# Performance work log

Measured on AMD Instinct MI355X. Metric: run time of the kernel, lower is better.

Reference implementation:

```python
import jax, jax.numpy as jnp
from jax import lax
import numpy as np

NEG_SLOPE = 0.01  # nn.LeakyReLU default


def conv1d(x, w, b, stride=1, padding=0, groups=1):
    # x: (N, C, L), w: (O, C//groups, K), torch Conv1d semantics
    y = lax.conv_general_dilated(
        x, w, window_strides=(stride,), padding=[(padding, padding)],
        dimension_numbers=('NCH', 'OIH', 'NCH'), feature_group_count=groups)
    return y + b[None, :, None]


def maxpool1d_ceil(x, k, s):
    # torch max_pool1d with ceil_mode=True: window may overhang right edge
    L = x.shape[-1]
    out_len = -(-(L - k) // s) + 1  # ceil((L-k)/s)+1
    pad = max(0, (out_len - 1) * s + k - L)
    xp = jnp.pad(x, ((0, 0), (0, 0), (0, pad)), constant_values=-jnp.inf)
    return lax.reduce_window(xp, -jnp.inf, lax.max, (1, 1, k), (1, 1, s), 'VALID')


def adaptive_maxpool1d(x, out_size):
    # Spatial_LSTM_block.get_adaptive_pool (ceil_mode=False default)
    L = x.shape[-1]
    s = L // out_size
    k = L - (out_size - 1) * s
    return lax.reduce_window(x, -jnp.inf, lax.max, (1, 1, k), (1, 1, s), 'VALID')


def lstm_last_h(xseq, w_ih, b_ih, w_hh, b_hh):
    # xseq: (T, B, F); PyTorch LSTMCell gate order: i, f, g, o
    B = xseq.shape[1]
    H = w_hh.shape[1]
    h0 = jnp.zeros((B, H), dtype=xseq.dtype)
    c0 = jnp.zeros((B, H), dtype=xseq.dtype)

    def step(carry, xt):
        h, c = carry
        g = xt @ w_ih.T + b_ih + h @ w_hh.T + b_hh  # (B, 4H)
        i, f, gg, o = jnp.split(g, 4, axis=-1)
        c = jax.nn.sigmoid(f) * c + jax.nn.sigmoid(i) * jnp.tanh(gg)
        h = jax.nn.sigmoid(o) * jnp.tanh(c)
        return (h, c), None

    (h, _), _ = lax.scan(step, (h0, c0), xseq)
    return h


def setup_inputs() -> dict:
    ks = jax.random.split(jax.random.key(0), 32)
    def rn(i, shape, s=0.05):
        return jax.random.normal(ks[i], shape, dtype=jnp.float32) * s
    return {
        'X': jax.random.normal(ks[0], (64, 16, 4096), dtype=jnp.float32),
        # depthwise conv: 16 -> 16*16=256, k=30, groups=16
        'w_dw': rn(1, (256, 1, 30)), 'b_dw': rn(2, (256,)),
        # pointwise conv: 256 -> 32, k=1
        'w_pw': rn(3, (32, 256, 1)), 'b_pw': rn(4, (32,)),
        # conv2: 32 -> 64, k=10
        'w_c2': rn(5, (64, 32, 10)), 'b_c2': rn(6, (64,)),
        # pyramid branch 0 (bin=300): conv 64->4 k=3 p=1, LSTMCell(4,64), Linear(64,1)
        'w_sc0': rn(7, (4, 64, 3)), 'b_sc0': rn(8, (4,)),
        'w_ih0': rn(9, (256, 4)), 'b_ih0': rn(10, (256,)),
        'w_hh0': rn(11, (256, 64)), 'b_hh0': rn(12, (256,)),
        'w_lin0': rn(13, (1, 64)), 'b_lin0': rn(14, (1,)),
        # pyramid branch 1 (bin=100)
        'w_sc1': rn(15, (4, 64, 3)), 'b_sc1': rn(16, (4,)),
        'w_ih1': rn(17, (256, 4)), 'b_ih1': rn(18, (256,)),
        'w_hh1': rn(19, (256, 64)), 'b_hh1': rn(20, (256,)),
        'w_lin1': rn(21, (1, 64)), 'b_lin1': rn(22, (1,)),
        # final head: Linear(len(bins)=2 -> 1), sigmoid
        'w_rul': rn(23, (1, 2)), 'b_rul': rn(24, (1,)),
    }


def reference(X, w_dw, b_dw, w_pw, b_pw, w_c2, b_c2,
              w_sc0, b_sc0, w_ih0, b_ih0, w_hh0, b_hh0, w_lin0, b_lin0,
              w_sc1, b_sc1, w_ih1, b_ih1, w_hh1, b_hh1, w_lin1, b_lin1,
              w_rul, b_rul):
    PYRAMID_BINS = (300, 100)
    x = conv1d(X, w_dw, b_dw, groups=16)            # (B, 256, 4067)
    x = conv1d(x, w_pw, b_pw)                        # (B, 32, 4067)
    x = jax.nn.leaky_relu(x, NEG_SLOPE)
    x = maxpool1d_ceil(x, 20, 5)                     # (B, 32, 811)
    x = conv1d(x, w_c2, b_c2)                        # (B, 64, 802)
    x = jax.nn.leaky_relu(x, NEG_SLOPE)
    branches = [
        (w_sc0, b_sc0, w_ih0, b_ih0, w_hh0, b_hh0, w_lin0, b_lin0),
        (w_sc1, b_sc1, w_ih1, b_ih1, w_hh1, b_hh1, w_lin1, b_lin1),
    ]
    outs = []
    for bin_size, (wsc, bsc, wih, bih, whh, bhh, wl, bl) in zip(PYRAMID_BINS, branches):
        xp = adaptive_maxpool1d(x, bin_size)          # (B, 64, bin)
        xc = jax.nn.leaky_relu(conv1d(xp, wsc, bsc, padding=1), NEG_SLOPE)  # (B, 4, bin)
        seq = jnp.transpose(xc, (2, 0, 1))            # (T, B, 4)
        h = lstm_last_h(seq, wih, bih, whh, bhh)      # (B, 64)
        outs.append(h @ wl.T + bl)                    # (B, 1)
    y = jnp.concatenate(outs, axis=1)                 # (B, 2)
    return jax.nn.sigmoid(y @ w_rul.T + b_rul)        # (B, 1)
```

## Files before the change

### kernel.cpp

```cpp
#include <hip/hip_runtime.h>
#include <cstddef>


typedef __attribute__((ext_vector_type(8))) short bf16x8;
typedef __attribute__((ext_vector_type(4))) float f32x4;
typedef unsigned int uint32;

#define LOG2E 1.4426950408889634f

__device__ __forceinline__ unsigned short f2bf(float f) {
    unsigned u = __float_as_uint(f);
    u += 0x7fffu + ((u >> 16) & 1u);
    return (unsigned short)(u >> 16);
}
__device__ __forceinline__ float bf2f(unsigned short h) {
    return __uint_as_float(((unsigned)h) << 16);
}
__device__ __forceinline__ float exp2_(float x) {
#if __has_builtin(__builtin_amdgcn_exp2f)
    return __builtin_amdgcn_exp2f(x);
#else
    return __expf(0.6931471805599453f * x);
#endif
}
__device__ __forceinline__ float rcp2(float x) {
    return __builtin_amdgcn_rcpf(1.0f + exp2_(x));
}
__device__ __forceinline__ float sigm(float x) {
    return __builtin_amdgcn_rcpf(1.0f + __expf(-x));
}
__device__ __forceinline__ float leaky(float v) { return v >= 0.0f ? v : 0.01f * v; }

__global__ void prep_kernel(const float* __restrict__ w_dw, const float* __restrict__ b_dw,
                            const float* __restrict__ w_pw, const float* __restrict__ b_pw,
                            unsigned short* __restrict__ Wp1, float* __restrict__ b_eff) {
    const int bid = blockIdx.x, tid = threadIdx.x;
    if (bid < 15) {
        const int kc = bid;
        for (int it = 0; it < 4; ++it) {
            int idx = tid + it * 256;
            int n = idx >> 5, kp = idx & 31;
            int ch = kp & 15, kappa = kc * 2 + (kp >> 4);
            float s = 0.f;
            for (int j = 0; j < 16; ++j)
                s += w_pw[n * 256 + ch * 16 + j] * w_dw[(ch * 16 + j) * 30 + kappa];
            Wp1[(kc * 32 + n) * 32 + kp] = f2bf(s);
        }
    } else if (tid < 32) {
        float s = b_pw[tid];
        for (int c = 0; c < 256; ++c) s += w_pw[tid * 256 + c] * b_dw[c];
        b_eff[tid] = s;
    }
}

__global__ __launch_bounds__(256) void conv1p_kernel(const float* __restrict__ X,
        const unsigned short* __restrict__ Wp1, const float* __restrict__ b_eff,
        unsigned short* __restrict__ S2b, int* __restrict__ cnt) {
    const int b = blockIdx.y, tx = blockIdx.x, tid = threadIdx.x;
    if (tx == 0 && b == 0 && tid == 0) *cnt = 0;
    const int l0 = tx * 160;
    __shared__ __align__(16) unsigned short Wl[480 * 40];
    __shared__ __align__(16) unsigned short U[192 * 33];
    unsigned short* Xt = U;
    {
        const int4* s4 = (const int4*)Wp1;
        for (int j = tid; j < 1920; j += 256)
            *(int4*)((uint32*)Wl + (j >> 2) * 20 + (j & 3) * 4) = s4[j];
    }
    for (int i = tid; i < 896; i += 256) {
        int ch = i / 56, p4 = (i - ch * 56) * 4;
        int l = l0 + p4;
        float4 v = {0.f, 0.f, 0.f, 0.f};
        const float* xrow = X + ((size_t)b * 16 + ch) * 4096;
        if (l + 3 < 4096 && p4 + 3 < 221) {
            v = *(const float4*)(xrow + l);
        } else {
            float* vv = (float*)&v;
#pragma unroll
            for (int e = 0; e < 4; ++e) {
                int p = p4 + e, le = l + e;
                vv[e] = (p < 221 && le < 4096) ? xrow[le] : 0.f;
            }
        }
        unsigned short* dst = Xt + p4 * 24 + ch;
        dst[0] = f2bf(v.x); dst[24] = f2bf(v.y); dst[48] = f2bf(v.z); dst[72] = f2bf(v.w);
    }
    __syncthreads();
    const int w = tid >> 6, lane = tid & 63, quad = lane >> 4, l16 = lane & 15;
    const int ki = quad >> 1, ch0 = (quad & 1) * 8;
    f32x4 acc[3][2];
#pragma unroll
    for (int mi = 0; mi < 3; ++mi)
#pragma unroll
        for (int nt = 0; nt < 2; ++nt) acc[mi][nt] = (f32x4){0.f, 0.f, 0.f, 0.f};
#pragma unroll
    for (int kc = 0; kc < 15; ++kc) {
        bf16x8 B0 = *(const bf16x8*)(Wl + (kc * 32 + l16) * 40 + quad * 8);
        bf16x8 B1 = *(const bf16x8*)(Wl + (kc * 32 + 16 + l16) * 40 + quad * 8);
#pragma unroll
        for (int mi = 0; mi < 3; ++mi) {
            int mrow = (w + mi * 4) * 16 + l16 + 2 * kc + ki;
            bf16x8 A = *(const bf16x8*)(Xt + mrow * 24 + ch0);
            acc[mi][0] = __builtin_amdgcn_mfma_f32_16x16x32_bf16(A, B0, acc[mi][0], 0, 0, 0);
            acc[mi][1] = __builtin_amdgcn_mfma_f32_16x16x32_bf16(A, B1, acc[mi][1], 0, 0, 0);
        }
    }
    __syncthreads();
    unsigned short* Ct = U;
#pragma unroll
    for (int mi = 0; mi < 3; ++mi) {
        int lrow = (w + mi * 4) * 16 + quad * 4;
#pragma unroll
        for (int nt = 0; nt < 2; ++nt) {
            int o = nt * 16 + l16;
            float be = b_eff[o];
#pragma unroll
            for (int r = 0; r < 4; ++r)
                Ct[(lrow + r) * 33 + o] = f2bf(leaky(acc[mi][nt][r] + be));
        }
    }
    __syncthreads();
    for (int idx = tid; idx < 1024; idx += 256) {
        int ti = idx >> 5, ch = idx & 31;
        int t = tx * 32 + ti;
        if (t < 811) {
            int pmax = 4067 - 5 * t; if (pmax > 20) pmax = 20;
            int pbase = 5 * ti;
            float m = bf2f(Ct[pbase * 33 + ch]);
            for (int p = 1; p < pmax; ++p) m = fmaxf(m, bf2f(Ct[(pbase + p) * 33 + ch]));
            S2b[((size_t)b * 32 + ch) * 812 + t] = f2bf(m);
        }
    }
}

__global__ __launch_bounds__(256) void conv2_kernel(const unsigned short* __restrict__ S2b,
        const float* __restrict__ w_c2, const float* __restrict__ b_c2,
        float* __restrict__ S3) {
    const int b = blockIdx.y, l0 = blockIdx.x * 64, tid = threadIdx.x;
    __shared__ __align__(16) unsigned short At[80 * 40];
    __shared__ __align__(16) unsigned short Wl[10 * 64 * 40];
    for (int pair = tid; pair < 2048; pair += 256) {
        int n = pair >> 5, kp = pair & 31;
        const float* src = w_c2 + n * 320 + kp * 10;
        unsigned short* dstc = Wl + n * 40 + kp;
#pragma unroll
        for (int kc = 0; kc < 10; ++kc) dstc[kc * 2560] = f2bf(src[kc]);
    }
    for (int i = tid; i < 2560; i += 256) {
        int ch = i / 80, p = i - ch * 80;
        int l = l0 + p;
        At[p * 40 + ch] = (p < 73 && l < 811)
            ? S2b[((size_t)b * 32 + ch) * 812 + l] : (unsigned short)0;
    }
    __syncthreads();
    const int w = tid >> 6, lane = tid & 63, quad = lane >> 4, l16 = lane & 15;
    const int mA = w * 16 + l16, ch0 = quad * 8;
    f32x4 acc[4];
#pragma unroll
    for (int nt = 0; nt < 4; ++nt) acc[nt] = (f32x4){0.f, 0.f, 0.f, 0.f};
#pragma unroll
    for (int kc = 0; kc < 10; ++kc) {
        bf16x8 A = *(const bf16x8*)(At + (mA + kc) * 40 + ch0);
#pragma unroll
        for (int nt = 0; nt < 4; ++nt) {
            bf16x8 Bf = *(const bf16x8*)(Wl + (kc * 64 + nt * 16 + l16) * 40 + quad * 8);
            acc[nt] = __builtin_amdgcn_mfma_f32_16x16x32_bf16(A, Bf, acc[nt], 0, 0, 0);
        }
    }
    const int lbase = l0 + w * 16 + quad * 4;
#pragma unroll
    for (int nt = 0; nt < 4; ++nt) {
        int o = nt * 16 + l16;
        float bc = b_c2[o];
#pragma unroll
        for (int r = 0; r < 4; ++r) {
            int l = lbase + r;
            if (l < 802) S3[((size_t)b * 64 + o) * 802 + l] = leaky(acc[nt][r] + bc);
        }
    }
}

__global__ __launch_bounds__(1024) void branch_kernel(const float* __restrict__ S3,
        const float* __restrict__ w_sc0, const float* __restrict__ b_sc0,
        const float* __restrict__ w_ih0, const float* __restrict__ b_ih0, const float* __restrict__ b_hh0,
        const float* __restrict__ w_sc1, const float* __restrict__ b_sc1,
        const float* __restrict__ w_ih1, const float* __restrict__ b_ih1, const float* __restrict__ b_hh1,
        float* __restrict__ Xg0, float* __restrict__ Xg1) {
    const int b = blockIdx.x, br = blockIdx.y;
    const int T = br ? 100 : 300;
    const float* w_sc = br ? w_sc1 : w_sc0;
    const float* b_sc = br ? b_sc1 : b_sc0;
    const float* w_ih = br ? w_ih1 : w_ih0;
    const float* b_ih = br ? b_ih1 : b_ih0;
    const float* b_hh = br ? b_hh1 : b_hh0;
    float* Xg = br ? Xg1 : Xg0;

    __shared__ float bufs[16][2][402];
    __shared__ unsigned short Ps[64][302];
    __shared__ float xcs[4][304];
    const int tid = threadIdx.x, wv = tid >> 6, lane = tid & 63;

    for (int ci = 0; ci < 4; ++ci) {
        const int c = wv * 4 + ci;
        const float* row = S3 + ((size_t)b * 64 + c) * 802;
        if (br == 0) {
            float* A = bufs[wv][0];
            float* B = bufs[wv][1];
            for (int it = 0; it < 7; ++it) {
                int q = lane + it * 64;
                if (q < 401) A[q] = fmaxf(row[2 * q], row[2 * q + 1]);
            }
            int len = 401;
#pragma unroll
            for (int sp = 1; sp <= 32; sp <<= 1) {
                int nl = len - sp;
                for (int it = 0; it < 7; ++it) {
                    int q = lane + it * 64;
                    if (q < nl) B[q] = fmaxf(A[q], A[q + sp]);
                }
                float* tmp = A; A = B; B = tmp; len = nl;
            }
            for (int it = 0; it < 5; ++it) {
                int t = lane + it * 64;
                if (t < 300) Ps[c][1 + t] = f2bf(fmaxf(A[t], A[t + 38]));
            }
            if (lane < 2) Ps[c][lane * 301] = 0;
        } else {
            for (int it = 0; it < 2; ++it) {
                int t = lane + it * 64;
                if (t < 100) {
                    float m = row[8 * t];
#pragma unroll
                    for (int p = 1; p < 10; ++p) m = fmaxf(m, row[8 * t + p]);
                    Ps[c][1 + t] = f2bf(m);
                }
            }
            if (lane < 2) Ps[c][lane * 101] = 0;
        }
    }
    __syncthreads();
    for (int i = tid; i < 4 * T; i += 1024) {
        int o = i / T, t = i - o * T;
        float sum = b_sc[o];
        const float* wvp = w_sc + o * 192;
        for (int c = 0; c < 64; ++c) {
            float p0 = bf2f(Ps[c][t]), p1 = bf2f(Ps[c][t + 1]), p2 = bf2f(Ps[c][t + 2]);
            sum += wvp[c * 3] * p0 + wvp[c * 3 + 1] * p1 + wvp[c * 3 + 2] * p2;
        }
        xcs[o][t] = leaky(sum);
    }
    __syncthreads();
    {
        const int n = tid & 255, tq = tid >> 8;
        const int g = n >> 6;
        const float sc = (g == 2) ? (-2.0f * LOG2E) : (-LOG2E);
        const float4 w4 = *(const float4*)(w_ih + n * 4);
        const float bias = b_ih[n] + b_hh[n];
        const int bt = b >> 2, q = b & 3;
        const int hidx = n & 63;
        const int wv2 = hidx >> 4, l16 = hidx & 15;
        const size_t off0 = ((((size_t)bt * 4 + wv2) * 4 + q) * 16 + l16) * 4 + g;
        for (int t = tq; t < T; t += 4) {
            float v = bias + w4.x * xcs[0][t] + w4.y * xcs[1][t]
                           + w4.z * xcs[2][t] + w4.w * xcs[3][t];
            Xg[(size_t)t * 16384 + off0] = sc * v;
        }
    }
}

#define HPAD 72
__global__ __launch_bounds__(256) void lstm_kernel(
    const float* __restrict__ Xg0, const float* __restrict__ Xg1,
    const float* __restrict__ Whh0, const float* __restrict__ Whh1,
    const float* __restrict__ wl0, const float* __restrict__ bl0,
    const float* __restrict__ wl1, const float* __restrict__ bl1,
    float* __restrict__ brbuf, int* __restrict__ cnt,
    const float* __restrict__ w_rul, const float* __restrict__ b_rul,
    float* __restrict__ out) {
    const int bt = blockIdx.x;
    const int br = blockIdx.y;
    const int T = (br == 0) ? 300 : 100;
    const float* Xg = (br == 0) ? Xg0 : Xg1;
    const float* Whh = (br == 0) ? Whh0 : Whh1;
    const float* wl = (br == 0) ? wl0 : wl1;
    const float* bl = (br == 0) ? bl0 : bl1;
    const float C2L = -2.0f * LOG2E;

    __shared__ __align__(16) unsigned short h_lds[2][16][HPAD];
    __shared__ int lastf;

    const int tid = threadIdx.x;
    const int w = tid >> 6, lane = tid & 63, quad = lane >> 4, l16 = lane & 15;
    const int hidx = w * 16 + l16;

    bf16x8 Bf[4][2];
#pragma unroll
    for (int g = 0; g < 4; ++g) {
        const int n = g * 64 + hidx;
        const float scg = (g == 2) ? (-2.0f * LOG2E) : (-LOG2E);
#pragma unroll
        for (int kc = 0; kc < 2; ++kc) {
            const float* src = Whh + n * 64 + kc * 32 + quad * 8;
            bf16x8 v;
#pragma unroll
            for (int j = 0; j < 8; ++j) v[j] = (short)f2bf(src[j] * scg);
            Bf[g][kc] = v;
        }
    }

    for (int i = tid; i < 2 * 16 * HPAD; i += 256) (&h_lds[0][0][0])[i] = 0;

    const float* xp = Xg + (((size_t)bt * 4 + w) * 4 + quad) * 64 + l16 * 4;

    f32x4 xb0 = *(const f32x4*)(xp);
    f32x4 xb1 = *(const f32x4*)(xp + 16384);

    float c0 = 0.f;

    __syncthreads();

    auto step = [&](int t, f32x4& xb) {
        const unsigned short* hrow = &h_lds[t & 1][l16][0];
        bf16x8 A0 = *(const bf16x8*)(hrow + quad * 8);
        bf16x8 A1 = *(const bf16x8*)(hrow + 32 + quad * 8);
        const f32x4 z = {0.f, 0.f, 0.f, 0.f};
        f32x4 ac[4];
#pragma unroll
        for (int g = 0; g < 4; ++g) {
            ac[g] = __builtin_amdgcn_mfma_f32_16x16x32_bf16(A0, Bf[g][0], z, 0, 0, 0);
            ac[g] = __builtin_amdgcn_mfma_f32_16x16x32_bf16(A1, Bf[g][1], ac[g], 0, 0, 0);
        }
        float iv = rcp2(ac[0][0] + xb[0]);
        float fv = rcp2(ac[1][0] + xb[1]);
        float gv = 2.0f * rcp2(ac[2][0] + xb[2]) - 1.0f;
        float ov = rcp2(ac[3][0] + xb[3]);
        if (t + 2 < T) xb = *(const f32x4*)(xp + (size_t)(t + 2) * 16384);
        float cs = fv * c0 + iv * gv;
        c0 = cs;
        float th = 2.0f * rcp2(cs * C2L) - 1.0f;
        h_lds[(t + 1) & 1][quad * 4][hidx] = f2bf(ov * th);
        __syncthreads();
    };

    for (int t = 0; t < T; t += 2) {
        step(t, xb0);
        step(t + 1, xb1);
    }

    if (tid < 4) {
        const unsigned short* hrow = &h_lds[0][tid * 4][0];
        float s = bl[0];
        for (int j = 0; j < 64; ++j) s += bf2f(hrow[j]) * wl[j];
        atomicExch(&brbuf[br * 64 + bt * 4 + tid], s);
    }
    __syncthreads();
    __threadfence();
    if (tid == 0) {
        int old = atomicAdd(cnt, 1);
        lastf = (old == 31);
    }
    __syncthreads();
    if (lastf) {
        __threadfence();
        if (tid < 64) {
            float v0 = atomicAdd(&brbuf[tid], 0.0f);
            float v1 = atomicAdd(&brbuf[64 + tid], 0.0f);
            float v = w_rul[0] * v0 + w_rul[1] * v1 + b_rul[0];
            out[tid] = sigm(v);
        }
    }
}

extern "C" void kernel_launch(void* const* d_in, const int* in_sizes, int n_in,
                              void* d_out, int out_size, void* d_ws, size_t ws_size,
                              hipStream_t stream) {
    const float* X     = (const float*)d_in[0];
    const float* w_dw  = (const float*)d_in[1];
    const float* b_dw  = (const float*)d_in[2];
    const float* w_pw  = (const float*)d_in[3];
    const float* b_pw  = (const float*)d_in[4];
    const float* w_c2  = (const float*)d_in[5];
    const float* b_c2  = (const float*)d_in[6];
    const float* w_sc0 = (const float*)d_in[7];
    const float* b_sc0 = (const float*)d_in[8];
    const float* w_ih0 = (const float*)d_in[9];
    const float* b_ih0 = (const float*)d_in[10];
    const float* w_hh0 = (const float*)d_in[11];
    const float* b_hh0 = (const float*)d_in[12];
    const float* w_l0  = (const float*)d_in[13];
    const float* b_l0  = (const float*)d_in[14];
    const float* w_sc1 = (const float*)d_in[15];
    const float* b_sc1 = (const float*)d_in[16];
    const float* w_ih1 = (const float*)d_in[17];
    const float* b_ih1 = (const float*)d_in[18];
    const float* w_hh1 = (const float*)d_in[19];
    const float* b_hh1 = (const float*)d_in[20];
    const float* w_l1  = (const float*)d_in[21];
    const float* b_l1  = (const float*)d_in[22];
    const float* w_rul = (const float*)d_in[23];
    const float* b_rul = (const float*)d_in[24];

    float* ws = (float*)d_ws;
    float* Xg0 = ws;
    float* Xg1 = ws + 4915200;
    unsigned short* S2b = (unsigned short*)(ws + 6553600);
    float* S3    = ws + 7385088;
    unsigned short* Wp1 = (unsigned short*)(ws + 10670080);
    float* b_eff = ws + 10677760;
    float* brbuf = ws + 10677792;
    int*   cnt   = (int*)(ws + 10677920);

    prep_kernel<<<16, 256, 0, stream>>>(w_dw, b_dw, w_pw, b_pw, Wp1, b_eff);
    conv1p_kernel<<<dim3(26, 64), 256, 0, stream>>>(X, Wp1, b_eff, S2b, cnt);
    conv2_kernel<<<dim3(13, 64), 256, 0, stream>>>(S2b, w_c2, b_c2, S3);
    branch_kernel<<<dim3(64, 2), 1024, 0, stream>>>(
        S3, w_sc0, b_sc0, w_ih0, b_ih0, b_hh0,
            w_sc1, b_sc1, w_ih1, b_ih1, b_hh1, Xg0, Xg1);
    lstm_kernel<<<dim3(16, 2), 256, 0, stream>>>(Xg0, Xg1, w_hh0, w_hh1,
                                                 w_l0, b_l0, w_l1, b_l1,
                                                 brbuf, cnt, w_rul, b_rul, (float*)d_out);
}
```

Measured before the change: 344.7 us.

## Interleave two independent batch tiles per LSTM block to hide MFMA latency

Each LSTM workgroup now carries two 4-sample batch tiles through the recurrence together. It issues their MFMAs interleaved so the two independent dependency chains overlap, and shares one barrier per timestep. The grid is halved to 8x2 blocks, the completion counter threshold drops accordingly, and the input-gate prefetch depth goes from 2 to 4 timesteps. This trades parallelism across CUs for better latency hiding within the serial recurrence, and raises register pressure.

```diff
diff --git a/kernel.cpp b/kernel.cpp
--- a/kernel.cpp
+++ b/kernel.cpp
@@ -277,7 +277,7 @@
     float* __restrict__ brbuf, int* __restrict__ cnt,
     const float* __restrict__ w_rul, const float* __restrict__ b_rul,
     float* __restrict__ out) {
-    const int bt = blockIdx.x;
+    const int btp = blockIdx.x;
     const int br = blockIdx.y;
     const int T = (br == 0) ? 300 : 100;
     const float* Xg = (br == 0) ? Xg0 : Xg1;
@@ -286,7 +286,7 @@
     const float* bl = (br == 0) ? bl0 : bl1;
     const float C2L = -2.0f * LOG2E;
 
-    __shared__ __align__(16) unsigned short h_lds[2][16][HPAD];
+    __shared__ __align__(16) unsigned short h_lds[2][2][16][HPAD];
     __shared__ int lastf;
 
     const int tid = threadIdx.x;
@@ -308,56 +308,79 @@
         }
     }
 
-    for (int i = tid; i < 2 * 16 * HPAD; i += 256) (&h_lds[0][0][0])[i] = 0;
-
-    const float* xp = Xg + (((size_t)bt * 4 + w) * 4 + quad) * 64 + l16 * 4;
-
-    f32x4 xb0 = *(const f32x4*)(xp);
-    f32x4 xb1 = *(const f32x4*)(xp + 16384);
-
-    float c0 = 0.f;
-
-    __syncthreads();
-
-    auto step = [&](int t, f32x4& xb) {
-        const unsigned short* hrow = &h_lds[t & 1][l16][0];
-        bf16x8 A0 = *(const bf16x8*)(hrow + quad * 8);
-        bf16x8 A1 = *(const bf16x8*)(hrow + 32 + quad * 8);
+    for (int i = tid; i < 2 * 2 * 16 * HPAD; i += 256) (&h_lds[0][0][0][0])[i] = 0;
+
+    const float* xp0 = Xg + ((((size_t)(2 * btp)) * 4 + w) * 4 + quad) * 64 + l16 * 4;
+    const float* xp1 = xp0 + 1024;
+
+    f32x4 xq0[4], xq1[4];
+#pragma unroll
+    for (int j = 0; j < 4; ++j) {
+        xq0[j] = *(const f32x4*)(xp0 + (size_t)j * 16384);
+        xq1[j] = *(const f32x4*)(xp1 + (size_t)j * 16384);
+    }
+
+    float c0 = 0.f, c1 = 0.f;
+
+    __syncthreads();
+
+    auto stepPair = [&](int t, f32x4& xa, f32x4& xb) {
+        const unsigned short* h0 = &h_lds[0][t & 1][l16][0];
+        const unsigned short* h1 = &h_lds[1][t & 1][l16][0];
+        bf16x8 A00 = *(const bf16x8*)(h0 + quad * 8);
+        bf16x8 A01 = *(const bf16x8*)(h0 + 32 + quad * 8);
+        bf16x8 A10 = *(const bf16x8*)(h1 + quad * 8);
+        bf16x8 A11 = *(const bf16x8*)(h1 + 32 + quad * 8);
         const f32x4 z = {0.f, 0.f, 0.f, 0.f};
-        f32x4 ac[4];
+        f32x4 ac0[4], ac1[4];
 #pragma unroll
         for (int g = 0; g < 4; ++g) {
-            ac[g] = __builtin_amdgcn_mfma_f32_16x16x32_bf16(A0, Bf[g][0], z, 0, 0, 0);
-            ac[g] = __builtin_amdgcn_mfma_f32_16x16x32_bf16(A1, Bf[g][1], ac[g], 0, 0, 0);
-        }
-        float iv = rcp2(ac[0][0] + xb[0]);
-        float fv = rcp2(ac[1][0] + xb[1]);
-        float gv = 2.0f * rcp2(ac[2][0] + xb[2]) - 1.0f;
-        float ov = rcp2(ac[3][0] + xb[3]);
-        if (t + 2 < T) xb = *(const f32x4*)(xp + (size_t)(t + 2) * 16384);
-        float cs = fv * c0 + iv * gv;
-        c0 = cs;
-        float th = 2.0f * rcp2(cs * C2L) - 1.0f;
-        h_lds[(t + 1) & 1][quad * 4][hidx] = f2bf(ov * th);
+            ac0[g] = __builtin_amdgcn_mfma_f32_16x16x32_bf16(A00, Bf[g][0], z, 0, 0, 0);
+            ac1[g] = __builtin_amdgcn_mfma_f32_16x16x32_bf16(A10, Bf[g][0], z, 0, 0, 0);
+            ac0[g] = __builtin_amdgcn_mfma_f32_16x16x32_bf16(A01, Bf[g][1], ac0[g], 0, 0, 0);
+            ac1[g] = __builtin_amdgcn_mfma_f32_16x16x32_bf16(A11, Bf[g][1], ac1[g], 0, 0, 0);
+        }
+        float i0 = rcp2(ac0[0][0] + xa[0]);
+        float f0 = rcp2(ac0[1][0] + xa[1]);
+        float g0 = 2.0f * rcp2(ac0[2][0] + xa[2]) - 1.0f;
+        float o0 = rcp2(ac0[3][0] + xa[3]);
+        float i1 = rcp2(ac1[0][0] + xb[0]);
+        float f1 = rcp2(ac1[1][0] + xb[1]);
+        float g1 = 2.0f * rcp2(ac1[2][0] + xb[2]) - 1.0f;
+        float o1 = rcp2(ac1[3][0] + xb[3]);
+        float cs0 = f0 * c0 + i0 * g0;  c0 = cs0;
+        float cs1 = f1 * c1 + i1 * g1;  c1 = cs1;
+        float th0 = 2.0f * rcp2(cs0 * C2L) - 1.0f;
+        float th1 = 2.0f * rcp2(cs1 * C2L) - 1.0f;
+        const int nb = (t + 1) & 1;
+        h_lds[0][nb][quad * 4][hidx] = f2bf(o0 * th0);
+        h_lds[1][nb][quad * 4][hidx] = f2bf(o1 * th1);
         __syncthreads();
     };
 
-    for (int t = 0; t < T; t += 2) {
-        step(t, xb0);
-        step(t + 1, xb1);
-    }
-
-    if (tid < 4) {
-        const unsigned short* hrow = &h_lds[0][tid * 4][0];
+    for (int t = 0; t < T; t += 4) {
+#pragma unroll
+        for (int j = 0; j < 4; ++j) {
+            stepPair(t + j, xq0[j], xq1[j]);
+            if (t + j + 4 < T) {
+                xq0[j] = *(const f32x4*)(xp0 + (size_t)(t + j + 4) * 16384);
+                xq1[j] = *(const f32x4*)(xp1 + (size_t)(t + j + 4) * 16384);
+            }
+        }
+    }
+
+    if (tid < 8) {
+        const int btl = tid >> 2, q = tid & 3;
+        const unsigned short* hrow = &h_lds[btl][0][q * 4][0];
         float s = bl[0];
         for (int j = 0; j < 64; ++j) s += bf2f(hrow[j]) * wl[j];
-        atomicExch(&brbuf[br * 64 + bt * 4 + tid], s);
+        atomicExch(&brbuf[br * 64 + btp * 8 + tid], s);
     }
     __syncthreads();
     __threadfence();
     if (tid == 0) {
         int old = atomicAdd(cnt, 1);
-        lastf = (old == 31);
+        lastf = (old == 15);
     }
     __syncthreads();
     if (lastf) {
@@ -416,7 +439,7 @@
     branch_kernel<<<dim3(64, 2), 1024, 0, stream>>>(
         S3, w_sc0, b_sc0, w_ih0, b_ih0, b_hh0,
             w_sc1, b_sc1, w_ih1, b_ih1, b_hh1, Xg0, Xg1);
-    lstm_kernel<<<dim3(16, 2), 256, 0, stream>>>(Xg0, Xg1, w_hh0, w_hh1,
-                                                 w_l0, b_l0, w_l1, b_l1,
-                                                 brbuf, cnt, w_rul, b_rul, (float*)d_out);
-}
+    lstm_kernel<<<dim3(8, 2), 256, 0, stream>>>(Xg0, Xg1, w_hh0, w_hh1,
+                                                w_l0, b_l0, w_l1, b_l1,
+                                                brbuf, cnt, w_rul, b_rul, (float*)d_out);
+}
```

Result: slower. 376.9 us (+9.4%).
